# Optimization experiments

Hardware: AMD Instinct MI355X
Metric: run time of the kernel (lower is better)

The kernel has to match this reference:

```python
import jax, jax.numpy as jnp
import numpy as np

N_HEAD, D_MODEL, D_HEAD = 16, 1024, 64
BSZ, SEQLEN = 2, 2048
ROPE_BASE = 10000.0


def _rope_tables(seqlen, d_head, base=ROPE_BASE):
    # freqs_cis = exp(i * t * theta_j), theta_j = base^(-2j/d_head)
    inv_freq = 1.0 / (base ** (np.arange(0, d_head, 2, dtype=np.float32) / d_head))
    t = np.arange(seqlen, dtype=np.float32)
    ang = np.outer(t, inv_freq)  # [S, d_head//2]
    return jnp.asarray(np.cos(ang)), jnp.asarray(np.sin(ang))


def setup_inputs() -> dict:
    key = jax.random.key(0)
    ks = jax.random.split(key, 5)
    x = jax.random.normal(ks[0], (BSZ, SEQLEN, D_MODEL), dtype=jnp.float32)
    freqs_cos, freqs_sin = _rope_tables(SEQLEN, D_HEAD)
    scale = 0.02
    # weights stored as (in, out) so projection is x @ w
    wq = jax.random.normal(ks[1], (D_MODEL, N_HEAD * D_HEAD), dtype=jnp.float32) * scale
    wk = jax.random.normal(ks[2], (D_MODEL, N_HEAD * D_HEAD), dtype=jnp.float32) * scale
    wv = jax.random.normal(ks[3], (D_MODEL, N_HEAD * D_HEAD), dtype=jnp.float32) * scale
    wo = jax.random.normal(ks[4], (N_HEAD * D_HEAD, D_MODEL), dtype=jnp.float32) * scale
    return {"x": x, "freqs_cos": freqs_cos, "freqs_sin": freqs_sin,
            "wq": wq, "wk": wk, "wv": wv, "wo": wo}


def _apply_rope(t, cos, sin):
    # t: [B, S, H, Dh]; complex pairs are consecutive elements (x0 + i*x1)
    B, S, H, Dh = t.shape
    tf = t.astype(jnp.float32).reshape(B, S, H, Dh // 2, 2)
    t0, t1 = tf[..., 0], tf[..., 1]
    c = cos[None, :, None, :]  # [1, S, 1, Dh//2]
    s = sin[None, :, None, :]
    o0 = t0 * c - t1 * s
    o1 = t0 * s + t1 * c
    return jnp.stack([o0, o1], axis=-1).reshape(B, S, H, Dh).astype(t.dtype)


def reference(x, freqs_cos, freqs_sin, wq, wk, wv, wo):
    B, S, _ = x.shape
    H, Dh = N_HEAD, D_HEAD
    q = jnp.einsum('bsd,de->bse', x, wq).reshape(B, S, H, Dh)
    k = jnp.einsum('bsd,de->bse', x, wk).reshape(B, S, H, Dh)
    v = jnp.einsum('bsd,de->bse', x, wv).reshape(B, S, H, Dh)
    q = _apply_rope(q, freqs_cos, freqs_sin)
    k = _apply_rope(k, freqs_cos, freqs_sin)
    # [B, H, S, Dh]
    q = q.transpose(0, 2, 1, 3)
    k = k.transpose(0, 2, 1, 3)
    v = v.transpose(0, 2, 1, 3)
    scores = jnp.einsum('bhqd,bhkd->bhqk', q, k) / jnp.sqrt(jnp.float32(Dh))
    probs = jax.nn.softmax(scores.astype(jnp.float32), axis=-1).astype(q.dtype)
    out = jnp.einsum('bhqk,bhkd->bhqd', probs, v)  # [B, H, S, Dh]
    out = out.transpose(0, 2, 1, 3).reshape(B, S, H * Dh)
    return jnp.einsum('bse,ed->bsd', out, wo)
```

## Files before the change

kernel.cpp:

```cpp
#include <hip/hip_runtime.h>
#include <math.h>

#define BSZ 2
#define SEQ 2048
#define NH 16
#define DH 64
#define DM 1024
#define HD 1024

typedef _Float16 h16;
typedef _Float16 half8 __attribute__((ext_vector_type(8)));
typedef _Float16 half4 __attribute__((ext_vector_type(4)));
typedef float f32x4 __attribute__((ext_vector_type(4)));

__device__ __forceinline__ f32x4 mfma16(half8 a, half8 b, f32x4 c) {
    return __builtin_amdgcn_mfma_f32_16x16x32_f16(a, b, c, 0, 0, 0);
}

__device__ __forceinline__ void async_copy16(h16* lds, const h16* g) {
    __builtin_amdgcn_global_load_lds(
        (const __attribute__((address_space(1))) unsigned int*)g,
        (__attribute__((address_space(3))) unsigned int*)lds, 16, 0, 0);
}

#define SWZ(cb, r) ((((cb) ^ ((r) & 7)) * 8))

#define PSA(r, c) ((r) * 128 + (((((c) >> 3) ^ ((r) & 15)) << 3) | ((c) & 7)))
#define OBA(r, c) ((r) * 64 + ((((c) >> 2) ^ ((r) & 15)) << 2))

#define EXP2(x) __builtin_amdgcn_exp2f(x)

__global__ __launch_bounds__(256) void prep_kernel(
    const float* __restrict__ x, const float* __restrict__ wq,
    const float* __restrict__ wk, const float* __restrict__ wv,
    const float* __restrict__ wo,
    h16* __restrict__ x16, h16* __restrict__ wt)
{
    const int z = blockIdx.z;
    const int t = threadIdx.x;
    if (z == 4) {
        int flat = blockIdx.y * 16 + blockIdx.x;
#pragma unroll
        for (int i = 0; i < 8; ++i) {
            int idx = flat * 16384 + i * 2048 + t * 8;
            float4 a = *(const float4*)&x[idx];
            float4 b = *(const float4*)&x[idx + 4];
            half8 o;
            o[0] = (h16)a.x; o[1] = (h16)a.y; o[2] = (h16)a.z; o[3] = (h16)a.w;
            o[4] = (h16)b.x; o[5] = (h16)b.y; o[6] = (h16)b.z; o[7] = (h16)b.w;
            *(half8*)&x16[idx] = o;
        }
        return;
    }
    const float* w = (z == 0) ? wq : (z == 1) ? wk : (z == 2) ? wv : wo;
    h16* ot = wt + (size_t)z * DM * DM;
    __shared__ float tile[64][68];
    const int k0 = blockIdx.y * 64, n0 = blockIdx.x * 64;
    const int r = t >> 2, c4 = (t & 3) * 16;
#pragma unroll
    for (int i = 0; i < 16; i += 4) {
        float4 v = *(const float4*)&w[(size_t)(k0 + r) * DM + n0 + c4 + i];
        tile[r][c4 + i + 0] = v.x; tile[r][c4 + i + 1] = v.y;
        tile[r][c4 + i + 2] = v.z; tile[r][c4 + i + 3] = v.w;
    }
    __syncthreads();
#pragma unroll
    for (int g = 0; g < 2; ++g) {
        half8 hh;
#pragma unroll
        for (int j = 0; j < 8; ++j)
            hh[j] = (h16)tile[c4 + g * 8 + j][r];
        *(half8*)&ot[(size_t)(n0 + r) * DM + k0 + c4 + g * 8] = hh;
    }
}

__global__ __launch_bounds__(512, 4) void qkv_kernel(
    const h16* __restrict__ x16, const h16* __restrict__ wt,
    const float* __restrict__ fcos, const float* __restrict__ fsin,
    h16* __restrict__ Q16, h16* __restrict__ K16, h16* __restrict__ VT16)
{
    const int id  = (blockIdx.z * 32 + blockIdx.y) * 8 + blockIdx.x;
    const int swz = (id & 7) * 96 + (id >> 3);
    const int z   = swz >> 8;
    const int m0  = ((swz >> 3) & 31) * 128;
    const int n0  = (swz & 7) * 128;

    const h16* __restrict__ bw = wt + (size_t)z * DM * DM;

    __shared__ h16 smem[32768];
    h16* Vt = smem;

    const int t  = threadIdx.x;
    const int w  = t >> 6, ln = t & 63;
    const int L  = ln & 15, U = ln >> 4;
    const int wm = (w & 3) * 32;
    const int wn = (w >> 2) * 64;

    const int sr  = ln >> 3;
    const int scb = (ln & 7) ^ sr;

    f32x4 acc[2][4];
#pragma unroll
    for (int i = 0; i < 2; ++i)
#pragma unroll
        for (int j = 0; j < 4; ++j) acc[i][j] = (f32x4)0.0f;

#pragma unroll
    for (int c = 0; c < 2; ++c) {
        int rb = w * 16 + c * 8;
        async_copy16(&smem[rb * 64],        &x16[(size_t)(m0 + rb + sr) * DM + scb * 8]);
        async_copy16(&smem[8192 + rb * 64], &bw [(size_t)(n0 + rb + sr) * DM + scb * 8]);
    }

    for (int k0 = 0; k0 < DM; k0 += 64) {
        const int buf = (k0 >> 6) & 1;
        h16* As = smem + buf * 16384;
        h16* Bs = As + 8192;

        asm volatile("s_waitcnt vmcnt(0)" ::: "memory");
        __builtin_amdgcn_s_barrier();
        __builtin_amdgcn_sched_barrier(0);

        if (k0 + 64 < DM) {
            h16* An = smem + (buf ^ 1) * 16384;
#pragma unroll
            for (int c = 0; c < 2; ++c) {
                int rb = w * 16 + c * 8;
                async_copy16(&An[rb * 64],
                             &x16[(size_t)(m0 + rb + sr) * DM + k0 + 64 + scb * 8]);
                async_copy16(&An[8192 + rb * 64],
                             &bw [(size_t)(n0 + rb + sr) * DM + k0 + 64 + scb * 8]);
            }
        }

        __builtin_amdgcn_s_setprio(1);
#pragma unroll
        for (int ks = 0; ks < 2; ++ks) {
            half8 af[2], bf[4];
#pragma unroll
            for (int mt = 0; mt < 2; ++mt)
                af[mt] = *(const half8*)&As[(wm + mt * 16 + L) * 64 + SWZ(ks * 4 + U, L)];
#pragma unroll
            for (int nt = 0; nt < 4; ++nt)
                bf[nt] = *(const half8*)&Bs[(wn + nt * 16 + L) * 64 + SWZ(ks * 4 + U, L)];
#pragma unroll
            for (int mt = 0; mt < 2; ++mt)
#pragma unroll
                for (int nt = 0; nt < 4; ++nt)
                    acc[mt][nt] = mfma16(bf[nt], af[mt], acc[mt][nt]);
        }
        __builtin_amdgcn_s_setprio(0);
    }

    const int b = m0 >> 11;
    const int sbase = m0 & 2047;

    if (z < 2) {
        const float sc = (z == 0) ? 0.125f * 1.44269504088896f : 1.0f;
#pragma unroll
        for (int mt = 0; mt < 2; ++mt) {
            int s = sbase + wm + mt * 16 + L;
            const float* ct = &fcos[s * 32];
            const float* st = &fsin[s * 32];
#pragma unroll
            for (int nt = 0; nt < 4; ++nt) {
                int nl = n0 + wn + nt * 16 + U * 4;
                int d = nl & 63, h = nl >> 6;
                int pd = d >> 1;
                float cv0 = ct[pd], sv0 = st[pd];
                float cv1 = ct[pd + 1], sv1 = st[pd + 1];
                float v0 = acc[mt][nt][0], v1 = acc[mt][nt][1];
                float v2 = acc[mt][nt][2], v3 = acc[mt][nt][3];
                float o0 = (v0 * cv0 - v1 * sv0) * sc;
                float o1 = (v0 * sv0 + v1 * cv0) * sc;
                float o2 = (v2 * cv1 - v3 * sv1) * sc;
                float o3 = (v2 * sv1 + v3 * cv1) * sc;
                size_t addr = ((size_t)(b * NH + h) * SEQ + s) * DH + d;
                half4 kk;
                kk[0] = (h16)o0; kk[1] = (h16)o1; kk[2] = (h16)o2; kk[3] = (h16)o3;
                if (z == 0) *(half4*)&Q16[addr] = kk;
                else        *(half4*)&K16[addr] = kk;
            }
        }
    } else {
        __syncthreads();
#pragma unroll
        for (int mt = 0; mt < 2; ++mt)
#pragma unroll
            for (int nt = 0; nt < 4; ++nt)
#pragma unroll
                for (int r = 0; r < 4; ++r) {
                    int nloc = wn + nt * 16 + U * 4 + r;
                    int sloc = wm + mt * 16 + L;
                    Vt[nloc * 136 + sloc] = (h16)acc[mt][nt][r];
                }
        __syncthreads();
#pragma unroll
        for (int i = 0; i < 4; ++i) {
            int c = i * 512 + t;
            int dl = c >> 4;
            int s8 = (c & 15) * 8;
            half8 vv = *(const half8*)&Vt[dl * 136 + s8];
            int n = n0 + dl;
            int d = n & 63, h = n >> 6;
            *(half8*)&VT16[((size_t)(b * NH + h) * DH + d) * SEQ + sbase + s8] = vv;
        }
    }
}

__global__ __launch_bounds__(512, 4) void attn_kernel(
    const h16* __restrict__ Q16, const h16* __restrict__ K16,
    const h16* __restrict__ VT16, h16* __restrict__ A16)
{
    __shared__ h16 smem[40960];
    h16* Ks  = smem;
    h16* VTs = smem + 8192;
    h16* Ps  = smem + 24576;
    float* lbuf = (float*)smem;
    float* Obuf = (float*)Ps;

    const int t = threadIdx.x, w = t >> 6, ln = t & 63;
    const int L = ln & 15, U = ln >> 4;
    const int pair = w >> 1, half = w & 1;
    const int qw = pair * 32, kh = half * 64;

    const int id  = blockIdx.y * 16 + blockIdx.x;
    const int swz = (id & 7) * 64 + (id >> 3);
    const int q0  = (swz & 15) * 128;
    const int bh  = swz >> 4;
    const size_t base = (size_t)bh * SEQ * DH;

    half8 qf[2][2];
#pragma unroll
    for (int qb = 0; qb < 2; ++qb)
#pragma unroll
        for (int ks = 0; ks < 2; ++ks)
            qf[qb][ks] = *(const half8*)&Q16[base + (size_t)(q0 + qw + qb * 16 + L) * DH + ks * 32 + U * 8];

    half8 one8;
#pragma unroll
    for (int i = 0; i < 8; ++i) one8[i] = (h16)1.0f;

    f32x4 O[4][2];
    f32x4 lsum[2];
#pragma unroll
    for (int dt = 0; dt < 4; ++dt)
#pragma unroll
        for (int qb = 0; qb < 2; ++qb) O[dt][qb] = (f32x4)0.0f;
    lsum[0] = (f32x4)0.0f;
    lsum[1] = (f32x4)0.0f;

    const int sr  = ln >> 3;
    const int scb = (ln & 7) ^ sr;

#pragma unroll
    for (int c = 0; c < 2; ++c) {
        int rv = (w * 2 + c) * 4;
        int c16 = (ln & 15) ^ ((rv + U) & 15);
        async_copy16(&VTs[rv * 128], &VT16[base + (size_t)(rv + U) * SEQ + c16 * 8]);
    }
#pragma unroll
    for (int c = 0; c < 2; ++c) {
        int rbk = c * 64 + w * 8;
        async_copy16(&Ks[rbk * 64], &K16[base + (size_t)(rbk + sr) * DH + scb * 8]);
    }

    for (int j0 = 0; j0 < SEQ; j0 += 128) {
        const int buf = (j0 >> 7) & 1;
        h16* VTcur = VTs + buf * 8192;

        asm volatile("s_waitcnt vmcnt(0)" ::: "memory");
        __builtin_amdgcn_s_barrier();
        __builtin_amdgcn_sched_barrier(0);

        if (j0 + 128 < SEQ) {
            h16* VTnxt = VTs + (buf ^ 1) * 8192;
#pragma unroll
            for (int c = 0; c < 2; ++c) {
                int rv = (w * 2 + c) * 4;
                int c16 = (ln & 15) ^ ((rv + U) & 15);
                async_copy16(&VTnxt[rv * 128],
                             &VT16[base + (size_t)(rv + U) * SEQ + (j0 + 128) + c16 * 8]);
            }
        }

        f32x4 S[4][2];
        __builtin_amdgcn_s_setprio(1);
#pragma unroll
        for (int nt = 0; nt < 4; ++nt) {
            S[nt][0] = (f32x4)0.0f;
            S[nt][1] = (f32x4)0.0f;
#pragma unroll
            for (int ks = 0; ks < 2; ++ks) {
                half8 kf = *(const half8*)&Ks[(kh + nt * 16 + L) * 64 + SWZ(ks * 4 + U, L)];
                S[nt][0] = mfma16(kf, qf[0][ks], S[nt][0]);
                S[nt][1] = mfma16(kf, qf[1][ks], S[nt][1]);
            }
        }
        __builtin_amdgcn_s_setprio(0);

        asm volatile("s_waitcnt lgkmcnt(0)" ::: "memory");
        __builtin_amdgcn_sched_barrier(0);
        __builtin_amdgcn_s_barrier();

        if (j0 + 128 < SEQ) {
#pragma unroll
            for (int c = 0; c < 2; ++c) {
                int rbk = c * 64 + w * 8;
                async_copy16(&Ks[rbk * 64],
                             &K16[base + (size_t)(j0 + 128 + rbk + sr) * DH + scb * 8]);
            }
        }

#pragma unroll
        for (int qb = 0; qb < 2; ++qb) {
            int prow = qw + qb * 16 + L;
#pragma unroll
            for (int nt = 0; nt < 4; ++nt) {
                half4 pq;
                pq[0] = (h16)EXP2(S[nt][qb][0]);
                pq[1] = (h16)EXP2(S[nt][qb][1]);
                pq[2] = (h16)EXP2(S[nt][qb][2]);
                pq[3] = (h16)EXP2(S[nt][qb][3]);
                *(half4*)&Ps[PSA(prow, kh + nt * 16 + U * 4)] = pq;
            }
        }

        half8 pf[2][2];
#pragma unroll
        for (int qb = 0; qb < 2; ++qb)
#pragma unroll
            for (int ks2 = 0; ks2 < 2; ++ks2)
                pf[qb][ks2] = *(const half8*)&Ps[PSA(qw + qb * 16 + L, kh + ks2 * 32 + U * 8)];

        __builtin_amdgcn_s_setprio(1);
#pragma unroll
        for (int dt = 0; dt < 4; ++dt)
#pragma unroll
            for (int ks2 = 0; ks2 < 2; ++ks2) {
                half8 vf = *(const half8*)&VTcur[(dt * 16 + L) * 128 + ((half * 8 + ks2 * 4 + U) ^ L) * 8];
                O[dt][0] = mfma16(vf, pf[0][ks2], O[dt][0]);
                O[dt][1] = mfma16(vf, pf[1][ks2], O[dt][1]);
            }
#pragma unroll
        for (int ks2 = 0; ks2 < 2; ++ks2) {
            lsum[0] = mfma16(one8, pf[0][ks2], lsum[0]);
            lsum[1] = mfma16(one8, pf[1][ks2], lsum[1]);
        }
        __builtin_amdgcn_s_setprio(0);
    }

    if (U == 0) {
        lbuf[w * 32 + L]      = lsum[0][0];
        lbuf[w * 32 + 16 + L] = lsum[1][0];
    }
    __syncthreads();
    const int pw = w ^ 1;
    float l_tot[2];
    l_tot[0] = lsum[0][0] + lbuf[pw * 32 + L];
    l_tot[1] = lsum[1][0] + lbuf[pw * 32 + 16 + L];

    if (half) {
#pragma unroll
        for (int qb = 0; qb < 2; ++qb)
#pragma unroll
            for (int dt = 0; dt < 4; ++dt)
                *(f32x4*)&Obuf[OBA(qw + qb * 16 + L, dt * 16 + U * 4)] = O[dt][qb];
    }
    __syncthreads();
    if (!half) {
        const int b = bh >> 4, hh = bh & 15;
#pragma unroll
        for (int qb = 0; qb < 2; ++qb) {
            float inv = 1.0f / l_tot[qb];
            int s = q0 + qw + qb * 16 + L;
#pragma unroll
            for (int dt = 0; dt < 4; ++dt) {
                f32x4 op = *(const f32x4*)&Obuf[OBA(qw + qb * 16 + L, dt * 16 + U * 4)];
                half4 o4;
#pragma unroll
                for (int r = 0; r < 4; ++r)
                    o4[r] = (h16)((O[dt][qb][r] + op[r]) * inv);
                *(half4*)&A16[(size_t)(b * SEQ + s) * HD + hh * DH + dt * 16 + U * 4] = o4;
            }
        }
    }
}

__global__ __launch_bounds__(512, 4) void oproj_kernel(
    const h16* __restrict__ A16, const h16* __restrict__ bw,
    float* __restrict__ out)
{
    __shared__ h16 smem[24576];

    const int id  = blockIdx.y * 16 + blockIdx.x;
    const int swz = (id & 7) * 64 + (id >> 3);
    const int n0  = (swz & 15) * 64;
    const int m0  = (swz >> 4) * 128;

    const int t  = threadIdx.x;
    const int w  = t >> 6, ln = t & 63;
    const int L  = ln & 15, U = ln >> 4;

    const int sr  = ln >> 3;
    const int scb = (ln & 7) ^ sr;

    f32x4 acc[4];
#pragma unroll
    for (int j = 0; j < 4; ++j) acc[j] = (f32x4)0.0f;

#pragma unroll
    for (int c = 0; c < 2; ++c) {
        int rb = w * 16 + c * 8;
        async_copy16(&smem[rb * 64], &A16[(size_t)(m0 + rb + sr) * DM + scb * 8]);
    }
    async_copy16(&smem[8192 + (w * 8) * 64], &bw[(size_t)(n0 + w * 8 + sr) * DM + scb * 8]);

    for (int k0 = 0; k0 < DM; k0 += 64) {
        const int buf = (k0 >> 6) & 1;
        h16* As = smem + buf * 12288;
        h16* Bs = As + 8192;

        asm volatile("s_waitcnt vmcnt(0)" ::: "memory");
        __builtin_amdgcn_s_barrier();
        __builtin_amdgcn_sched_barrier(0);

        if (k0 + 64 < DM) {
            h16* An = smem + (buf ^ 1) * 12288;
#pragma unroll
            for (int c = 0; c < 2; ++c) {
                int rb = w * 16 + c * 8;
                async_copy16(&An[rb * 64],
                             &A16[(size_t)(m0 + rb + sr) * DM + k0 + 64 + scb * 8]);
            }
            async_copy16(&An[8192 + (w * 8) * 64],
                         &bw[(size_t)(n0 + w * 8 + sr) * DM + k0 + 64 + scb * 8]);
        }

        __builtin_amdgcn_s_setprio(1);
#pragma unroll
        for (int ks = 0; ks < 2; ++ks) {
            half8 af, bf[4];
            af = *(const half8*)&As[(w * 16 + L) * 64 + SWZ(ks * 4 + U, L)];
#pragma unroll
            for (int nt = 0; nt < 4; ++nt)
                bf[nt] = *(const half8*)&Bs[(nt * 16 + L) * 64 + SWZ(ks * 4 + U, L)];
#pragma unroll
            for (int nt = 0; nt < 4; ++nt)
                acc[nt] = mfma16(af, bf[nt], acc[nt]);
        }
        __builtin_amdgcn_s_setprio(0);
    }

#pragma unroll
    for (int nt = 0; nt < 4; ++nt)
#pragma unroll
        for (int r = 0; r < 4; ++r) {
            int row = m0 + w * 16 + U * 4 + r;
            int col = n0 + nt * 16 + L;
            out[(size_t)row * DM + col] = acc[nt][r];
        }
}

extern "C" void kernel_launch(void* const* d_in, const int* in_sizes, int n_in,
                              void* d_out, int out_size, void* d_ws, size_t ws_size,
                              hipStream_t stream)
{
    const float* x    = (const float*)d_in[0];
    const float* fcos = (const float*)d_in[1];
    const float* fsin = (const float*)d_in[2];
    const float* wq   = (const float*)d_in[3];
    const float* wk   = (const float*)d_in[4];
    const float* wv   = (const float*)d_in[5];
    const float* wo   = (const float*)d_in[6];
    float* out = (float*)d_out;

    const size_t M4 = (size_t)4 * 1024 * 1024;
    h16* x16  = (h16*)d_ws;
    h16* wt   = x16 + M4;
    h16* Q16  = wt + M4;
    h16* K16  = Q16 + M4;
    h16* VT16 = K16 + M4;
    h16* A16  = VT16 + M4;

    prep_kernel<<<dim3(16, 16, 5), 256, 0, stream>>>(x, wq, wk, wv, wo, x16, wt);
    qkv_kernel<<<dim3(8, 32, 3), 512, 0, stream>>>(x16, wt, fcos, fsin,
                                                   Q16, K16, VT16);
    attn_kernel<<<dim3(16, 32), 512, 0, stream>>>(Q16, K16, VT16, A16);
    oproj_kernel<<<dim3(16, 32), 512, 0, stream>>>(A16, wt + 3 * (size_t)DM * DM, out);
}
```

Before: 179.3 us.

## Transpose P fragments in registers with permlane swaps; double-buffer K

Replaces the LDS round trip for the softmax probability tile (write P to shared memory, then read back in MFMA B-operand layout) with register-level permlane32/permlane16 swaps that rearrange the packed fp16 values directly into the operand layout. This drops the Ps buffer and the mid-iteration barrier and lgkmcnt wait that guarded K reuse. K is now double-buffered alongside V and prefetched at the top of each iteration. The change cuts LDS traffic and synchronisation per tile, at the cost of extra cross-lane permute instructions and a fallback path built on ds_swizzle if the builtins are missing.

Result: slower. 183.2 us (+2.2%).

```diff
diff --git a/kernel.cpp b/kernel.cpp
--- a/kernel.cpp
+++ b/kernel.cpp
@@ -12,6 +12,9 @@
 typedef _Float16 half8 __attribute__((ext_vector_type(8)));
 typedef _Float16 half4 __attribute__((ext_vector_type(4)));
 typedef float f32x4 __attribute__((ext_vector_type(4)));
+typedef unsigned int u32;
+typedef unsigned int u32x2v __attribute__((ext_vector_type(2)));
+typedef unsigned int u32x4v __attribute__((ext_vector_type(4)));
 
 __device__ __forceinline__ f32x4 mfma16(half8 a, half8 b, f32x4 c) {
     return __builtin_amdgcn_mfma_f32_16x16x32_f16(a, b, c, 0, 0, 0);
@@ -25,10 +28,43 @@
 
 #define SWZ(cb, r) ((((cb) ^ ((r) & 7)) * 8))
 
-#define PSA(r, c) ((r) * 128 + (((((c) >> 3) ^ ((r) & 15)) << 3) | ((c) & 7)))
 #define OBA(r, c) ((r) * 64 + ((((c) >> 2) ^ ((r) & 15)) << 2))
 
 #define EXP2(x) __builtin_amdgcn_exp2f(x)
+
+__device__ __forceinline__ u32 pack2(float a, float b) {
+    h16 lo = (h16)a, hi = (h16)b;
+    return (u32)__builtin_bit_cast(unsigned short, lo) |
+           ((u32)__builtin_bit_cast(unsigned short, hi) << 16);
+}
+
+__device__ __forceinline__ void pl32swap(u32& a, u32& b) {
+#if __has_builtin(__builtin_amdgcn_permlane32_swap)
+    u32x2v r = __builtin_amdgcn_permlane32_swap(a, b, false, false);
+    a = r.x; b = r.y;
+#else
+    u32 sa = __builtin_amdgcn_ds_swizzle(a, 0x801F);
+    u32 sb = __builtin_amdgcn_ds_swizzle(b, 0x801F);
+    bool hi = (threadIdx.x & 32) != 0;
+    u32 na = hi ? sb : a;
+    u32 nb = hi ? b : sa;
+    a = na; b = nb;
+#endif
+}
+
+__device__ __forceinline__ void pl16swap(u32& a, u32& b) {
+#if __has_builtin(__builtin_amdgcn_permlane16_swap)
+    u32x2v r = __builtin_amdgcn_permlane16_swap(a, b, false, false);
+    a = r.x; b = r.y;
+#else
+    u32 sa = __builtin_amdgcn_ds_swizzle(a, 0x401F);
+    u32 sb = __builtin_amdgcn_ds_swizzle(b, 0x401F);
+    bool hi = (threadIdx.x & 16) != 0;
+    u32 na = hi ? sb : a;
+    u32 nb = hi ? b : sa;
+    a = na; b = nb;
+#endif
+}
 
 __global__ __launch_bounds__(256) void prep_kernel(
     const float* __restrict__ x, const float* __restrict__ wq,
@@ -212,12 +248,9 @@
     const h16* __restrict__ Q16, const h16* __restrict__ K16,
     const h16* __restrict__ VT16, h16* __restrict__ A16)
 {
-    __shared__ h16 smem[40960];
-    h16* Ks  = smem;
-    h16* VTs = smem + 8192;
-    h16* Ps  = smem + 24576;
-    float* lbuf = (float*)smem;
-    float* Obuf = (float*)Ps;
+    __shared__ h16 smem[32768];
+    float* lbuf = (float*)(smem + 16384);
+    float* Obuf = (float*)smem;
 
     const int t = threadIdx.x, w = t >> 6, ln = t & 63;
     const int L = ln & 15, U = ln >> 4;
@@ -255,31 +288,40 @@
 
 #pragma unroll
     for (int c = 0; c < 2; ++c) {
+        int rbk = c * 64 + w * 8;
+        async_copy16(&smem[rbk * 64], &K16[base + (size_t)(rbk + sr) * DH + scb * 8]);
+    }
+#pragma unroll
+    for (int c = 0; c < 2; ++c) {
         int rv = (w * 2 + c) * 4;
         int c16 = (ln & 15) ^ ((rv + U) & 15);
-        async_copy16(&VTs[rv * 128], &VT16[base + (size_t)(rv + U) * SEQ + c16 * 8]);
-    }
-#pragma unroll
-    for (int c = 0; c < 2; ++c) {
-        int rbk = c * 64 + w * 8;
-        async_copy16(&Ks[rbk * 64], &K16[base + (size_t)(rbk + sr) * DH + scb * 8]);
+        async_copy16(&smem[16384 + rv * 128], &VT16[base + (size_t)(rv + U) * SEQ + c16 * 8]);
     }
 
     for (int j0 = 0; j0 < SEQ; j0 += 128) {
         const int buf = (j0 >> 7) & 1;
-        h16* VTcur = VTs + buf * 8192;
-
+        h16* Kcur  = smem + buf * 8192;
+        h16* VTcur = smem + 16384 + buf * 8192;
+
+        __builtin_amdgcn_sched_barrier(0);
         asm volatile("s_waitcnt vmcnt(0)" ::: "memory");
         __builtin_amdgcn_s_barrier();
         __builtin_amdgcn_sched_barrier(0);
 
         if (j0 + 128 < SEQ) {
-            h16* VTnxt = VTs + (buf ^ 1) * 8192;
+            h16* Knxt  = smem + (buf ^ 1) * 8192;
+            h16* Vnxt  = smem + 16384 + (buf ^ 1) * 8192;
+#pragma unroll
+            for (int c = 0; c < 2; ++c) {
+                int rbk = c * 64 + w * 8;
+                async_copy16(&Knxt[rbk * 64],
+                             &K16[base + (size_t)(j0 + 128 + rbk + sr) * DH + scb * 8]);
+            }
 #pragma unroll
             for (int c = 0; c < 2; ++c) {
                 int rv = (w * 2 + c) * 4;
                 int c16 = (ln & 15) ^ ((rv + U) & 15);
-                async_copy16(&VTnxt[rv * 128],
+                async_copy16(&Vnxt[rv * 128],
                              &VT16[base + (size_t)(rv + U) * SEQ + (j0 + 128) + c16 * 8]);
             }
         }
@@ -292,46 +334,41 @@
             S[nt][1] = (f32x4)0.0f;
 #pragma unroll
             for (int ks = 0; ks < 2; ++ks) {
-                half8 kf = *(const half8*)&Ks[(kh + nt * 16 + L) * 64 + SWZ(ks * 4 + U, L)];
+                half8 kf = *(const half8*)&Kcur[(kh + nt * 16 + L) * 64 + SWZ(ks * 4 + U, L)];
                 S[nt][0] = mfma16(kf, qf[0][ks], S[nt][0]);
                 S[nt][1] = mfma16(kf, qf[1][ks], S[nt][1]);
             }
         }
         __builtin_amdgcn_s_setprio(0);
 
-        asm volatile("s_waitcnt lgkmcnt(0)" ::: "memory");
-        __builtin_amdgcn_sched_barrier(0);
-        __builtin_amdgcn_s_barrier();
-
-        if (j0 + 128 < SEQ) {
-#pragma unroll
-            for (int c = 0; c < 2; ++c) {
-                int rbk = c * 64 + w * 8;
-                async_copy16(&Ks[rbk * 64],
-                             &K16[base + (size_t)(j0 + 128 + rbk + sr) * DH + scb * 8]);
-            }
-        }
-
+        half8 pf[2][2];
 #pragma unroll
         for (int qb = 0; qb < 2; ++qb) {
-            int prow = qw + qb * 16 + L;
-#pragma unroll
-            for (int nt = 0; nt < 4; ++nt) {
-                half4 pq;
-                pq[0] = (h16)EXP2(S[nt][qb][0]);
-                pq[1] = (h16)EXP2(S[nt][qb][1]);
-                pq[2] = (h16)EXP2(S[nt][qb][2]);
-                pq[3] = (h16)EXP2(S[nt][qb][3]);
-                *(half4*)&Ps[PSA(prow, kh + nt * 16 + U * 4)] = pq;
-            }
-        }
-
-        half8 pf[2][2];
-#pragma unroll
-        for (int qb = 0; qb < 2; ++qb)
-#pragma unroll
-            for (int ks2 = 0; ks2 < 2; ++ks2)
-                pf[qb][ks2] = *(const half8*)&Ps[PSA(qw + qb * 16 + L, kh + ks2 * 32 + U * 8)];
+            u32 X[2][2][2];
+#pragma unroll
+            for (int k5 = 0; k5 < 2; ++k5)
+#pragma unroll
+                for (int p = 0; p < 2; ++p) {
+                    u32 a = pack2(EXP2(S[k5 * 2 + 0][qb][2 * p]),
+                                  EXP2(S[k5 * 2 + 0][qb][2 * p + 1]));
+                    u32 b = pack2(EXP2(S[k5 * 2 + 1][qb][2 * p]),
+                                  EXP2(S[k5 * 2 + 1][qb][2 * p + 1]));
+                    pl32swap(a, b);
+                    X[k5][0][p] = a; X[k5][1][p] = b;
+                }
+#pragma unroll
+            for (int k5 = 0; k5 < 2; ++k5) {
+                u32x4v uv;
+#pragma unroll
+                for (int p = 0; p < 2; ++p) {
+                    u32 a = X[k5][0][p], b = X[k5][1][p];
+                    pl16swap(a, b);
+                    uv[p]     = a;
+                    uv[2 + p] = b;
+                }
+                pf[qb][k5] = __builtin_bit_cast(half8, uv);
+            }
+        }
 
         __builtin_amdgcn_s_setprio(1);
 #pragma unroll
```
